# Kernel optimization log

Hardware: AMD Instinct MI355X
Metric: run time of the kernel (lower is better)

## Reference

```python
import jax, jax.numpy as jnp
import numpy as np

B, L, C, D = 4, 2048, 64, 4


def setup_inputs() -> dict:
    key = jax.random.key(0)
    k1, k2, k3, k4 = jax.random.split(key, 4)
    # |A| kept < ~0.92 so the length-2048 recurrence stays bounded
    A_re = jax.random.uniform(k1, (B, L, C, D), jnp.float32, -0.65, 0.65)
    A_im = jax.random.uniform(k2, (B, L, C, D), jnp.float32, -0.65, 0.65)
    X_re = jax.random.normal(k3, (B, L, C, D, D), jnp.float32)
    X_im = jax.random.normal(k4, (B, L, C, D, D), jnp.float32)
    return {"A_re": A_re, "A_im": A_im, "X_re": X_re, "X_im": X_im}


def _combine(c1, c2):
    # first-order linear recurrence combine: (a, x) o (b, y) = (b*a, b*x + y)
    a1, x1 = c1
    a2, x2 = c2
    return a2 * a1, a2 * x1 + x2


def reference(A_re, A_im, X_re, X_im):
    # Diagonal complex pscan: Y[t] = A[t] * Y[t-1] + X[t], elementwise,
    # with diagonal A [B,L,C,D] broadcast over the trailing D dim of X [B,L,C,D,D]
    A = (A_re + 1j * A_im).astype(jnp.complex64)[..., None]  # [B,L,C,D,1]
    X = (X_re + 1j * X_im).astype(jnp.complex64)             # [B,L,C,D,D]
    _, Y = jax.lax.associative_scan(_combine, (A, X), axis=1)
    # return real view [B,L,C,D,D,2] (real, imag) like torch.view_as_real
    return jnp.stack([Y.real, Y.imag], axis=-1)
```

## Files before the change

kernel.cpp:

```cpp
#include <hip/hip_runtime.h>

#define BB 4
#define LL 2048
#define CC 64
#define DD 4
#define NN (CC * DD * DD)
#define AN (CC * DD)
#define TPB 512
#define N4PB 4
#define NSEGS (TPB / N4PB)
#define TT (LL / NSEGS)

typedef float f32x4 __attribute__((ext_vector_type(4)));

__global__ __launch_bounds__(512, 2) void pscan_onepass3(
    const float* __restrict__ A_re, const float* __restrict__ A_im,
    const f32x4* __restrict__ X_re4, const f32x4* __restrict__ X_im4,
    f32x4* __restrict__ out4) {
  const int sid = (blockIdx.x & 7) * 32 + (blockIdx.x >> 3);
  const int b    = sid >> 6;
  const int n4g  = sid & 63;
  const int tid  = threadIdx.x;
  const int n4l  = tid & (N4PB - 1);
  const int tseg = tid >> 2;
  const int n4   = n4g * N4PB + n4l;
  const int t0   = tseg * TT;
  const int base = (b * LL + t0) * AN + n4;

  float ar[TT], ai[TT];
  f32x4 xr[TT], xi[TT];
  float p_re = 1.f, p_im = 0.f;
  float s_re[4] = {0.f, 0.f, 0.f, 0.f};
  float s_im[4] = {0.f, 0.f, 0.f, 0.f};
#pragma unroll
  for (int t = 0; t < TT; ++t) {
    const float are = A_re[base + t * AN];
    const float aim = A_im[base + t * AN];
    ar[t] = are; ai[t] = aim;
    xr[t] = X_re4[base + t * AN];
    xi[t] = X_im4[base + t * AN];
    const float npre = are * p_re - aim * p_im;
    const float npim = are * p_im + aim * p_re;
    p_re = npre; p_im = npim;
#pragma unroll
    for (int j = 0; j < 4; ++j) {
      const float nsre = are * s_re[j] - aim * s_im[j] + xr[t][j];
      const float nsim = are * s_im[j] + aim * s_re[j] + xi[t][j];
      s_re[j] = nsre; s_im[j] = nsim;
    }
  }

  __shared__ float lds[TPB * 11];
  const int q = tid * 11;
  lds[q + 0] = p_re; lds[q + 1] = p_im;
#pragma unroll
  for (int j = 0; j < 4; ++j) { lds[q + 2 + j] = s_re[j]; lds[q + 6 + j] = s_im[j]; }

  float vp_re = p_re, vp_im = p_im;
  float vs_re[4], vs_im[4];
#pragma unroll
  for (int j = 0; j < 4; ++j) { vs_re[j] = s_re[j]; vs_im[j] = s_im[j]; }

  for (int d = 1; d < NSEGS; d <<= 1) {
    __syncthreads();
    float wp_re = 1.f, wp_im = 0.f;
    float ws_re[4] = {0.f, 0.f, 0.f, 0.f};
    float ws_im[4] = {0.f, 0.f, 0.f, 0.f};
    if (tseg >= d) {
      const int q2 = q - d * (N4PB * 11);
      wp_re = lds[q2 + 0]; wp_im = lds[q2 + 1];
#pragma unroll
      for (int j = 0; j < 4; ++j) { ws_re[j] = lds[q2 + 2 + j]; ws_im[j] = lds[q2 + 6 + j]; }
    }
    __syncthreads();
    if (tseg >= d) {
      const float np_re = vp_re * wp_re - vp_im * wp_im;
      const float np_im = vp_re * wp_im + vp_im * wp_re;
#pragma unroll
      for (int j = 0; j < 4; ++j) {
        const float ns_re = vp_re * ws_re[j] - vp_im * ws_im[j] + vs_re[j];
        const float ns_im = vp_re * ws_im[j] + vp_im * ws_re[j] + vs_im[j];
        vs_re[j] = ns_re; vs_im[j] = ns_im;
      }
      vp_re = np_re; vp_im = np_im;
      lds[q + 0] = vp_re; lds[q + 1] = vp_im;
#pragma unroll
      for (int j = 0; j < 4; ++j) { lds[q + 2 + j] = vs_re[j]; lds[q + 6 + j] = vs_im[j]; }
    }
  }
  __syncthreads();

  float y_re[4] = {0.f, 0.f, 0.f, 0.f};
  float y_im[4] = {0.f, 0.f, 0.f, 0.f};
  if (tseg > 0) {
    const int qc = q - N4PB * 11;
#pragma unroll
    for (int j = 0; j < 4; ++j) { y_re[j] = lds[qc + 2 + j]; y_im[j] = lds[qc + 6 + j]; }
  }

  const int ob = (b * LL + t0) * (2 * AN) + n4 * 2;
#pragma unroll
  for (int t = 0; t < TT; ++t) {
    const float are = ar[t], aim = ai[t];
#pragma unroll
    for (int j = 0; j < 4; ++j) {
      const float ny_re = are * y_re[j] - aim * y_im[j] + xr[t][j];
      const float ny_im = are * y_im[j] + aim * y_re[j] + xi[t][j];
      y_re[j] = ny_re; y_im[j] = ny_im;
    }
    f32x4 o0 = {y_re[0], y_im[0], y_re[1], y_im[1]};
    f32x4 o1 = {y_re[2], y_im[2], y_re[3], y_im[3]};
    out4[ob + t * (2 * AN)]     = o0;
    out4[ob + t * (2 * AN) + 1] = o1;
  }
}

extern "C" void kernel_launch(void* const* d_in, const int* in_sizes, int n_in,
                              void* d_out, int out_size, void* d_ws, size_t ws_size,
                              hipStream_t stream) {
  const float* A_re  = (const float*)d_in[0];
  const float* A_im  = (const float*)d_in[1];
  const f32x4* X_re4 = (const f32x4*)d_in[2];
  const f32x4* X_im4 = (const f32x4*)d_in[3];
  f32x4* out4 = (f32x4*)d_out;
  (void)d_ws; (void)ws_size;

  const int blocks = BB * (AN / N4PB);
  pscan_onepass3<<<blocks, TPB, 0, stream>>>(A_re, A_im, X_re4, X_im4, out4);
}
```

Baseline: 142.2 us.

## Split sequence into two halves across blocks with flag-based carry lookback

```diff
diff --git a/kernel.cpp b/kernel.cpp
--- a/kernel.cpp
+++ b/kernel.cpp
@@ -4,31 +4,36 @@
 #define LL 2048
 #define CC 64
 #define DD 4
-#define NN (CC * DD * DD)
 #define AN (CC * DD)
 #define TPB 512
 #define N4PB 4
 #define NSEGS (TPB / N4PB)
-#define TT (LL / NSEGS)
+#define TT 8
+#define HALF (NSEGS * TT)
+#define NBG (BB * (AN / N4PB))
 
 typedef float f32x4 __attribute__((ext_vector_type(4)));
 
-__global__ __launch_bounds__(512, 2) void pscan_onepass3(
+__global__ __launch_bounds__(TPB, 4) void pscan_lookback(
     const float* __restrict__ A_re, const float* __restrict__ A_im,
     const f32x4* __restrict__ X_re4, const f32x4* __restrict__ X_im4,
+    float* __restrict__ ws_data, unsigned int* __restrict__ flags,
     f32x4* __restrict__ out4) {
-  const int sid = (blockIdx.x & 7) * 32 + (blockIdx.x >> 3);
-  const int b    = sid >> 6;
-  const int n4g  = sid & 63;
+  const int xcd = blockIdx.x & 7;
+  const int idx = blockIdx.x >> 3;
+  const int h   = idx >> 5;
+  const int bg  = xcd * 32 + (idx & 31);
+  const int b   = bg >> 6;
+  const int n4g = bg & 63;
   const int tid  = threadIdx.x;
   const int n4l  = tid & (N4PB - 1);
   const int tseg = tid >> 2;
   const int n4   = n4g * N4PB + n4l;
-  const int t0   = tseg * TT;
-  const int base = (b * LL + t0) * AN + n4;
+  const int tg0  = h * HALF + tseg * TT;
+  const int base = (b * LL + tg0) * AN + n4;
 
   float ar[TT], ai[TT];
-  f32x4 xr[TT], xi[TT];
+  float xre[TT][4], xim[TT][4];
   float p_re = 1.f, p_im = 0.f;
   float s_re[4] = {0.f, 0.f, 0.f, 0.f};
   float s_im[4] = {0.f, 0.f, 0.f, 0.f};
@@ -37,20 +42,31 @@
     const float are = A_re[base + t * AN];
     const float aim = A_im[base + t * AN];
     ar[t] = are; ai[t] = aim;
-    xr[t] = X_re4[base + t * AN];
-    xi[t] = X_im4[base + t * AN];
+    const f32x4 tr = X_re4[base + t * AN];
+    const f32x4 ti = X_im4[base + t * AN];
+#pragma unroll
+    for (int j = 0; j < 4; ++j) { xre[t][j] = tr[j]; xim[t][j] = ti[j]; }
     const float npre = are * p_re - aim * p_im;
     const float npim = are * p_im + aim * p_re;
     p_re = npre; p_im = npim;
 #pragma unroll
     for (int j = 0; j < 4; ++j) {
-      const float nsre = are * s_re[j] - aim * s_im[j] + xr[t][j];
-      const float nsim = are * s_im[j] + aim * s_re[j] + xi[t][j];
+      const float nsre = are * s_re[j] - aim * s_im[j] + xre[t][j];
+      const float nsim = are * s_im[j] + aim * s_re[j] + xim[t][j];
       s_re[j] = nsre; s_im[j] = nsim;
     }
   }
+#pragma unroll
+  for (int t = 0; t < TT; ++t) {
+    asm volatile("" : "+v"(ar[t]), "+v"(ai[t]),
+                      "+v"(xre[t][0]), "+v"(xre[t][1]),
+                      "+v"(xre[t][2]), "+v"(xre[t][3]),
+                      "+v"(xim[t][0]), "+v"(xim[t][1]),
+                      "+v"(xim[t][2]), "+v"(xim[t][3]));
+  }
 
   __shared__ float lds[TPB * 11];
+  __shared__ float eLDS[32];
   const int q = tid * 11;
   lds[q + 0] = p_re; lds[q + 1] = p_im;
 #pragma unroll
@@ -90,22 +106,55 @@
   }
   __syncthreads();
 
-  float y_re[4] = {0.f, 0.f, 0.f, 0.f};
-  float y_im[4] = {0.f, 0.f, 0.f, 0.f};
+  if (h == 0 && tseg == NSEGS - 1) {
+    float* wd = ws_data + bg * 32 + n4l * 8;
+#pragma unroll
+    for (int j = 0; j < 4; ++j) { wd[j * 2] = vs_re[j]; wd[j * 2 + 1] = vs_im[j]; }
+    __hip_atomic_fetch_add(&flags[bg], 1u, __ATOMIC_RELEASE, __HIP_MEMORY_SCOPE_AGENT);
+  }
+
+  float lp_re = 1.f, lp_im = 0.f;
+  float ls_re[4] = {0.f, 0.f, 0.f, 0.f};
+  float ls_im[4] = {0.f, 0.f, 0.f, 0.f};
   if (tseg > 0) {
     const int qc = q - N4PB * 11;
+    lp_re = lds[qc + 0]; lp_im = lds[qc + 1];
 #pragma unroll
-    for (int j = 0; j < 4; ++j) { y_re[j] = lds[qc + 2 + j]; y_im[j] = lds[qc + 6 + j]; }
+    for (int j = 0; j < 4; ++j) { ls_re[j] = lds[qc + 2 + j]; ls_im[j] = lds[qc + 6 + j]; }
   }
 
-  const int ob = (b * LL + t0) * (2 * AN) + n4 * 2;
+  float e_re[4] = {0.f, 0.f, 0.f, 0.f};
+  float e_im[4] = {0.f, 0.f, 0.f, 0.f};
+  if (h == 1) {
+    if (tid < 32) {
+      while (__hip_atomic_load(&flags[bg], __ATOMIC_ACQUIRE, __HIP_MEMORY_SCOPE_AGENT) < 4u) {
+        __builtin_amdgcn_s_sleep(1);
+      }
+      eLDS[tid] = ws_data[bg * 32 + tid];
+    }
+    __syncthreads();
+#pragma unroll
+    for (int j = 0; j < 4; ++j) {
+      e_re[j] = eLDS[n4l * 8 + j * 2];
+      e_im[j] = eLDS[n4l * 8 + j * 2 + 1];
+    }
+  }
+
+  float y_re[4], y_im[4];
+#pragma unroll
+  for (int j = 0; j < 4; ++j) {
+    y_re[j] = ls_re[j] + lp_re * e_re[j] - lp_im * e_im[j];
+    y_im[j] = ls_im[j] + lp_re * e_im[j] + lp_im * e_re[j];
+  }
+
+  const int ob = (b * LL + tg0) * (2 * AN) + n4 * 2;
 #pragma unroll
   for (int t = 0; t < TT; ++t) {
     const float are = ar[t], aim = ai[t];
 #pragma unroll
     for (int j = 0; j < 4; ++j) {
-      const float ny_re = are * y_re[j] - aim * y_im[j] + xr[t][j];
-      const float ny_im = are * y_im[j] + aim * y_re[j] + xi[t][j];
+      const float ny_re = are * y_re[j] - aim * y_im[j] + xre[t][j];
+      const float ny_im = are * y_im[j] + aim * y_re[j] + xim[t][j];
       y_re[j] = ny_re; y_im[j] = ny_im;
     }
     f32x4 o0 = {y_re[0], y_im[0], y_re[1], y_im[1]};
@@ -123,8 +172,12 @@
   const f32x4* X_re4 = (const f32x4*)d_in[2];
   const f32x4* X_im4 = (const f32x4*)d_in[3];
   f32x4* out4 = (f32x4*)d_out;
-  (void)d_ws; (void)ws_size;
 
-  const int blocks = BB * (AN / N4PB);
-  pscan_onepass3<<<blocks, TPB, 0, stream>>>(A_re, A_im, X_re4, X_im4, out4);
+  float* ws_data = (float*)d_ws;
+  unsigned int* flags = (unsigned int*)((char*)d_ws + NBG * 32 * sizeof(float));
+  hipMemsetAsync(flags, 0, NBG * sizeof(unsigned int), stream);
+
+  const int blocks = 2 * NBG;
+  pscan_lookback<<<blocks, TPB, 0, stream>>>(A_re, A_im, X_re4, X_im4,
+                                             ws_data, flags, out4);
 }
```

Result: slower. 186.0 us (+30.8%).

## Stage half of X in LDS and reload the rest after the scan

Applied to the files above, without the earlier changes.

```diff
diff --git a/kernel.cpp b/kernel.cpp
--- a/kernel.cpp
+++ b/kernel.cpp
@@ -4,16 +4,149 @@
 #define LL 2048
 #define CC 64
 #define DD 4
-#define NN (CC * DD * DD)
 #define AN (CC * DD)
 #define TPB 512
 #define N4PB 4
 #define NSEGS (TPB / N4PB)
 #define TT (LL / NSEGS)
+#define TH (TT / 2)
+#define SCAN_FLOATS (TPB * 11)
+#define SHMEM_BYTES (SCAN_FLOATS * 4 + 2 * TH * TPB * 16)
 
 typedef float f32x4 __attribute__((ext_vector_type(4)));
 
-__global__ __launch_bounds__(512, 2) void pscan_onepass3(
+__global__ __launch_bounds__(TPB, 2) void pscan_v10(
+    const float* __restrict__ A_re, const float* __restrict__ A_im,
+    const f32x4* __restrict__ X_re4, const f32x4* __restrict__ X_im4,
+    f32x4* __restrict__ out4) {
+  extern __shared__ char smem[];
+  float* lds  = (float*)smem;
+  f32x4* stR  = (f32x4*)(smem + SCAN_FLOATS * 4);
+  f32x4* stI  = stR + TH * TPB;
+
+  const int sid = (blockIdx.x & 7) * 32 + (blockIdx.x >> 3);
+  const int b    = sid >> 6;
+  const int n4g  = sid & 63;
+  const int tid  = threadIdx.x;
+  const int n4l  = tid & (N4PB - 1);
+  const int tseg = tid >> 2;
+  const int n4   = n4g * N4PB + n4l;
+  const int t0   = tseg * TT;
+  const int base = (b * LL + t0) * AN + n4;
+
+  float ar[TT], ai[TT];
+  float p_re = 1.f, p_im = 0.f;
+  float s_re[4] = {0.f, 0.f, 0.f, 0.f};
+  float s_im[4] = {0.f, 0.f, 0.f, 0.f};
+#pragma unroll
+  for (int t = 0; t < TT; ++t) {
+    const float are = A_re[base + t * AN];
+    const float aim = A_im[base + t * AN];
+    ar[t] = are; ai[t] = aim;
+    const f32x4 xr = X_re4[base + t * AN];
+    const f32x4 xi = X_im4[base + t * AN];
+    if (t < TH) { stR[t * TPB + tid] = xr; stI[t * TPB + tid] = xi; }
+    const float npre = are * p_re - aim * p_im;
+    const float npim = are * p_im + aim * p_re;
+    p_re = npre; p_im = npim;
+#pragma unroll
+    for (int j = 0; j < 4; ++j) {
+      const float nsre = are * s_re[j] - aim * s_im[j] + xr[j];
+      const float nsim = are * s_im[j] + aim * s_re[j] + xi[j];
+      s_re[j] = nsre; s_im[j] = nsim;
+    }
+  }
+
+  const int q = tid * 11;
+  lds[q + 0] = p_re; lds[q + 1] = p_im;
+#pragma unroll
+  for (int j = 0; j < 4; ++j) { lds[q + 2 + j] = s_re[j]; lds[q + 6 + j] = s_im[j]; }
+
+  float vp_re = p_re, vp_im = p_im;
+  float vs_re[4], vs_im[4];
+#pragma unroll
+  for (int j = 0; j < 4; ++j) { vs_re[j] = s_re[j]; vs_im[j] = s_im[j]; }
+
+  for (int d = 1; d < NSEGS; d <<= 1) {
+    __syncthreads();
+    float wp_re = 1.f, wp_im = 0.f;
+    float ws_re[4] = {0.f, 0.f, 0.f, 0.f};
+    float ws_im[4] = {0.f, 0.f, 0.f, 0.f};
+    if (tseg >= d) {
+      const int q2 = q - d * (N4PB * 11);
+      wp_re = lds[q2 + 0]; wp_im = lds[q2 + 1];
+#pragma unroll
+      for (int j = 0; j < 4; ++j) { ws_re[j] = lds[q2 + 2 + j]; ws_im[j] = lds[q2 + 6 + j]; }
+    }
+    __syncthreads();
+    if (tseg >= d) {
+      const float np_re = vp_re * wp_re - vp_im * wp_im;
+      const float np_im = vp_re * wp_im + vp_im * wp_re;
+#pragma unroll
+      for (int j = 0; j < 4; ++j) {
+        const float ns_re = vp_re * ws_re[j] - vp_im * ws_im[j] + vs_re[j];
+        const float ns_im = vp_re * ws_im[j] + vp_im * ws_re[j] + vs_im[j];
+        vs_re[j] = ns_re; vs_im[j] = ns_im;
+      }
+      vp_re = np_re; vp_im = np_im;
+      lds[q + 0] = vp_re; lds[q + 1] = vp_im;
+#pragma unroll
+      for (int j = 0; j < 4; ++j) { lds[q + 2 + j] = vs_re[j]; lds[q + 6 + j] = vs_im[j]; }
+    }
+  }
+  __syncthreads();
+
+  float y_re[4] = {0.f, 0.f, 0.f, 0.f};
+  float y_im[4] = {0.f, 0.f, 0.f, 0.f};
+  if (tseg > 0) {
+    const int qc = q - N4PB * 11;
+#pragma unroll
+    for (int j = 0; j < 4; ++j) { y_re[j] = lds[qc + 2 + j]; y_im[j] = lds[qc + 6 + j]; }
+  }
+
+  f32x4 xr2[TT - TH], xi2[TT - TH];
+#pragma unroll
+  for (int t = TH; t < TT; ++t) {
+    xr2[t - TH] = X_re4[base + t * AN];
+    xi2[t - TH] = X_im4[base + t * AN];
+  }
+
+  const int ob = (b * LL + t0) * (2 * AN) + n4 * 2;
+#pragma unroll
+  for (int t = 0; t < TH; ++t) {
+    const f32x4 xr = stR[t * TPB + tid];
+    const f32x4 xi = stI[t * TPB + tid];
+    const float are = ar[t], aim = ai[t];
+#pragma unroll
+    for (int j = 0; j < 4; ++j) {
+      const float ny_re = are * y_re[j] - aim * y_im[j] + xr[j];
+      const float ny_im = are * y_im[j] + aim * y_re[j] + xi[j];
+      y_re[j] = ny_re; y_im[j] = ny_im;
+    }
+    f32x4 o0 = {y_re[0], y_im[0], y_re[1], y_im[1]};
+    f32x4 o1 = {y_re[2], y_im[2], y_re[3], y_im[3]};
+    out4[ob + t * (2 * AN)]     = o0;
+    out4[ob + t * (2 * AN) + 1] = o1;
+  }
+#pragma unroll
+  for (int t = TH; t < TT; ++t) {
+    const f32x4 xr = xr2[t - TH];
+    const f32x4 xi = xi2[t - TH];
+    const float are = ar[t], aim = ai[t];
+#pragma unroll
+    for (int j = 0; j < 4; ++j) {
+      const float ny_re = are * y_re[j] - aim * y_im[j] + xr[j];
+      const float ny_im = are * y_im[j] + aim * y_re[j] + xi[j];
+      y_re[j] = ny_re; y_im[j] = ny_im;
+    }
+    f32x4 o0 = {y_re[0], y_im[0], y_re[1], y_im[1]};
+    f32x4 o1 = {y_re[2], y_im[2], y_re[3], y_im[3]};
+    out4[ob + t * (2 * AN)]     = o0;
+    out4[ob + t * (2 * AN) + 1] = o1;
+  }
+}
+
+__global__ __launch_bounds__(TPB, 2) void pscan_onepass3(
     const float* __restrict__ A_re, const float* __restrict__ A_im,
     const f32x4* __restrict__ X_re4, const f32x4* __restrict__ X_im4,
     f32x4* __restrict__ out4) {
@@ -126,5 +259,18 @@
   (void)d_ws; (void)ws_size;
 
   const int blocks = BB * (AN / N4PB);
-  pscan_onepass3<<<blocks, TPB, 0, stream>>>(A_re, A_im, X_re4, X_im4, out4);
+
+  static int v10_ok = -1;
+  if (v10_ok < 0) {
+    hipError_t e = hipFuncSetAttribute(
+        reinterpret_cast<const void*>(pscan_v10),
+        hipFuncAttributeMaxDynamicSharedMemorySize, (int)SHMEM_BYTES);
+    v10_ok = (e == hipSuccess) ? 1 : 0;
+  }
+
+  if (v10_ok) {
+    pscan_v10<<<blocks, TPB, SHMEM_BYTES, stream>>>(A_re, A_im, X_re4, X_im4, out4);
+  } else {
+    pscan_onepass3<<<blocks, TPB, 0, stream>>>(A_re, A_im, X_re4, X_im4, out4);
+  }
 }
```

Result: slower. 146.2 us (+2.9%).
